# Optimization experiments

Hardware: AMD Instinct MI355X
Metric: run time of the kernel (lower is better)

## Reference

```python
import jax, jax.numpy as jnp
import numpy as np

K = 11  # masked conv3d kernel size

def mask_A(k):
    # mask type 'A': flattened (i,j,t) positions with current_id < k^3//2 + 1
    # (current_id starts at 1) -> first k^3//2 positions are 1.
    m = (np.arange(k ** 3) < (k ** 3) // 2).astype(np.float32).reshape(k, k, k)
    return jnp.asarray(m)

def conv3d(x, w, b, pad):
    out = jax.lax.conv_general_dilated(
        x, w, window_strides=(1, 1, 1), padding=[(pad, pad)] * 3,
        dimension_numbers=('NCDHW', 'OIDHW', 'NCDHW'))
    return out + b[None, :, None, None, None]

def conv2d(x, w, b, pad):
    out = jax.lax.conv_general_dilated(
        x, w, window_strides=(1, 1), padding=[(pad, pad)] * 2,
        dimension_numbers=('NCHW', 'OIHW', 'NCHW'))
    return out + b[None, :, None, None]

def pconv(x, w, b):
    # 1x1x1 conv3d as channel GEMM; w: [O, C]
    return jnp.einsum('bcdhw,oc->bodhw', x, w) + b[None, :, None, None, None]

def _phi(z):
    return 0.5 * (1.0 + jax.lax.erf(z / jnp.sqrt(2.0).astype(z.dtype)))

def setup_inputs() -> dict:
    key = jax.random.key(0)
    ks = jax.random.split(key, 12)
    M = 192
    B, H, W = 1, 48, 48
    s = 0.02
    x = jax.random.normal(ks[0], (B, M, H, W), jnp.float32)
    hyper = jax.random.normal(ks[1], (B, 2 * M, H, W), jnp.float32)
    W3 = s * jax.random.normal(ks[2], (M, 2 * M, 3, 3), jnp.float32)
    b3 = jnp.zeros((M,), jnp.float32)
    W1 = s * jax.random.normal(ks[3], (24, 1, K, K, K), jnp.float32)
    b1 = jnp.zeros((24,), jnp.float32)
    Wa = s * jax.random.normal(ks[4], (48, 25), jnp.float32)
    ba = jnp.zeros((48,), jnp.float32)
    Wb = s * jax.random.normal(ks[5], (96, 48), jnp.float32)
    bb = jnp.zeros((96,), jnp.float32)
    Wc = s * jax.random.normal(ks[6], (9, 96), jnp.float32)
    bc = jnp.zeros((9,), jnp.float32)
    return {"x": x, "hyper": hyper, "W3": W3, "b3": b3, "W1": W1, "b1": b1,
            "Wa": Wa, "ba": ba, "Wb": Wb, "bb": bb, "Wc": Wc, "bc": bc}

def reference(x, hyper, W3, b3, W1, b1, Wa, ba, Wb, bb, Wc, bc):
    # x: [B,M,H,W], hyper: [B,2M,H,W]
    x5 = x[:, None]                                   # [B,1,M,H,W]
    h = conv2d(hyper, W3, b3, 1)[:, None]             # [B,1,M,H,W]
    W1m = W1 * mask_A(K)[None, None]                  # causal mask re-applied each fwd
    x1 = conv3d(x5, W1m, b1, 5)                       # [B,24,M,H,W]
    t = jnp.concatenate([x1, h], axis=1)              # [B,25,M,H,W]
    t = jax.nn.relu(pconv(t, Wa, ba))                 # [B,48,M,H,W]
    t = jax.nn.relu(pconv(t, Wb, bb))                 # [B,96,M,H,W]
    out = pconv(t, Wc, bc)                            # [B,9,M,H,W]
    # 3-component weighted Gaussian entropy model
    mu = out[:, 0:3]
    sc = out[:, 3:6]
    sc = jnp.abs(jnp.where(sc == 0.0, 1e-9, sc))
    w = jax.nn.softmax(out[:, 6:9], axis=1)
    xe = x[:, None]                                   # [B,1,M,H,W]
    lik = jnp.abs(_phi((xe + 0.5 - mu) / sc) - _phi((xe - 0.5 - mu) / sc))
    p3 = jnp.sum(w * lik, axis=1)                     # [B,M,H,W]
    return (p3, out)
```

## Files before the change

kernel.cpp:

```cpp
#include <hip/hip_runtime.h>
#include <hip/hip_fp16.h>
#include <math.h>

#define HW    2304
#define NPOS  442368

typedef _Float16 f16x8 __attribute__((ext_vector_type(8)));
typedef __fp16   h16x2 __attribute__((ext_vector_type(2)));
typedef float    f32x4 __attribute__((ext_vector_type(4)));

__device__ __forceinline__ float phi_f(float z) {
    return 0.5f * (1.0f + erff(z * 0.70710678118654752f));
}
__device__ __forceinline__ unsigned short f2h(float v) {
    _Float16 h = (_Float16)v;
    return *reinterpret_cast<unsigned short*>(&h);
}
__device__ __forceinline__ unsigned int pk2(float a, float b) {
    return (unsigned int)f2h(a) | ((unsigned int)f2h(b) << 16);
}
__device__ __forceinline__ unsigned int pkrtz(float a, float b) {
    h16x2 h = __builtin_amdgcn_cvt_pkrtz(a, b);
    return *reinterpret_cast<unsigned int*>(&h);
}
__device__ __forceinline__ unsigned int bperm(int idx4, unsigned int v) {
    return (unsigned int)__builtin_amdgcn_ds_bpermute(idx4, (int)v);
}

__global__ __launch_bounds__(256) void prep_hyperTp(const float* __restrict__ hyper,
                                                    unsigned short* __restrict__ hyperTp) {
    __shared__ float s[32][33];
    const int bx = blockIdx.x;
    const int pt = bx % 79, it = bx / 79;
    const int tid = threadIdx.x;
    const int c = tid & 31, r = tid >> 5;
    const int pp = pt * 32 + c;
    const int yp = pp / 50, xp = pp % 50;
    const bool inter = (pp < 2500) && yp >= 1 && yp <= 48 && xp >= 1 && xp <= 48;
    const int src = inter ? ((yp - 1) * 48 + (xp - 1)) : 0;
#pragma unroll
    for (int i = 0; i < 4; ++i) {
        int icl = r + i * 8;
        s[icl][c] = inter ? hyper[(size_t)(it * 32 + icl) * HW + src] : 0.f;
    }
    __syncthreads();
#pragma unroll
    for (int i = 0; i < 4; ++i) {
        int pl = r + i * 8;
        int pp2 = pt * 32 + pl;
        if (pp2 < 2500)
            hyperTp[(size_t)pp2 * 384 + it * 32 + c] = f2h(s[c][pl]);
    }
}

__global__ __launch_bounds__(256) void prep_apack(const float* __restrict__ W3,
                                                  unsigned short* __restrict__ apack) {
    int idx = blockIdx.x * 256 + threadIdx.x;
    int j = idx & 7;
    int l = (idx >> 3) & 63;
    int rest = idx >> 9;
    int t = rest % 9; rest /= 9;
    int c = rest % 12; int T = rest / 12;
    int oc = T * 16 + (l & 15);
    int ic = c * 32 + (l >> 4) * 8 + j;
    apack[idx] = f2h(W3[((size_t)oc * 384 + ic) * 9 + t]);
}

__global__ __launch_bounds__(256) void prep_rest(const float* __restrict__ W1,
                                                 const float* __restrict__ Wa,
                                                 const float* __restrict__ ba,
                                                 const float* __restrict__ b1,
                                                 const float* __restrict__ Wb,
                                                 const float* __restrict__ bb,
                                                 const float* __restrict__ Wc,
                                                 const float* __restrict__ xg,
                                                 unsigned short* __restrict__ pk,
                                                 unsigned short* __restrict__ xhp) {
    const int bx = blockIdx.x;
    if (bx < 160) {
        int idx = bx * 256 + threadIdx.x;
        float v = 0.f;
        if (idx < 31744) {
            int j = idx & 7, lane = (idx >> 3) & 63, s = (idx >> 9) & 1, c = idx >> 10;
            int q = lane >> 4;
            int oc = s * 16 + (lane & 15);
            int r = 2 * c + (q >> 1), h = q & 1, kw = 8 * h + j;
            if (oc < 24 && r < 61 && kw < 11) {
                int kd = r / 11, kh = r % 11;
                int tap = kd * 121 + kh * 11 + kw;
                if (tap < 665) v = W1[oc * 1331 + tap];
            }
        } else if (idx < 33280) {
            int i2 = idx - 31744;
            int j = i2 & 7, lane = (i2 >> 3) & 63, t = i2 >> 9;
            int m = t * 16 + (lane & 15), k = (lane >> 4) * 8 + j;
            if (k < 25) v = Wa[m * 25 + k];
            else if (k == 25) {
                float s = ba[m];
                for (int c = 0; c < 24; ++c) s += Wa[m * 25 + c] * b1[c];
                v = s;
            }
        } else if (idx < 39424) {
            int i3 = idx - 33280;
            int j = i3 & 7, lane = (i3 >> 3) & 63, k2 = (i3 >> 9) & 1, s = i3 >> 10;
            int m = s * 16 + (lane & 15), ch = k2 * 32 + (lane >> 4) * 8 + j;
            if (ch < 48) v = Wb[m * 48 + ch];
            else if (ch == 48) v = bb[m];
        } else {
            int i4 = idx - 39424;
            int j = i4 & 7, lane = (i4 >> 3) & 63, k3 = i4 >> 9;
            int m = lane & 15, ch = k3 * 32 + (lane >> 4) * 8 + j;
            if (m < 9) v = Wc[m * 96 + ch];
        }
        pk[idx] = f2h(v);
    } else {
        int idx = (bx - 160) * 256 + threadIdx.x;
        if (idx >= 187456) return;
        int si = idx * 4;
        int zp = si / 3712, rem = si - zp * 3712;
        int yp = rem >> 6, xp0 = rem & 63;
        float f[4];
#pragma unroll
        for (int k = 0; k < 4; ++k) {
            int xp = xp0 + k;
            bool in = zp >= 5 && zp < 197 && yp >= 5 && yp < 53 && xp >= 5 && xp < 53;
            f[k] = in ? xg[(size_t)(zp - 5) * HW + (yp - 5) * 48 + (xp - 5)] : 0.f;
        }
        *(uint2*)&xhp[si] = make_uint2(pk2(f[0], f[1]), pk2(f[2], f[3]));
    }
}

__global__ __launch_bounds__(256, 4) void fused3(const unsigned short* __restrict__ xhp,
                                                 const unsigned short* __restrict__ pk,
                                                 const unsigned short* __restrict__ hyperTp,
                                                 const unsigned short* __restrict__ apack,
                                                 const float* __restrict__ b3,
                                                 const float* __restrict__ xg,
                                                 const float* __restrict__ bc,
                                                 float* __restrict__ out) {
    __shared__ __align__(16) unsigned short P[6656];
    __shared__ __align__(16) float htile[256];
    __shared__ __align__(16) unsigned short WU[9216];

    const int tid = threadIdx.x, w = tid >> 6, lane = tid & 63;
    const int n = lane & 15, q = lane >> 4;
    const int bx = blockIdx.x;
    const int x0 = (bx % 12) * 4, y0 = ((bx / 12) % 12) * 4;
    const int T = bx / 144, d0 = T * 16;

    float* hpart = (float*)WU;

#pragma unroll
    for (int k = 0; k < 3; ++k) {
        int idx = tid + k * 256;
        if (idx < 588) {
            int row = idx >> 1, half = idx & 1;
            int py = row / 21, pz = row - py * 21;
            const uint4* src = (const uint4*)(xhp + ((size_t)(d0 + pz) * 58 + (y0 + py)) * 64
                                              + x0 + half * 8);
            *(uint4*)&P[row * 16 + half * 8] = *src;
        }
    }

    {
        const int pp = (y0 + (n >> 2)) * 50 + x0 + (n & 3);
        const size_t bbase = (size_t)pp * 384 + q * 8;
        f32x4 hc[3];
#pragma unroll
        for (int cc = 0; cc < 3; ++cc) {
            const int c = w * 3 + cc;
            const unsigned short* ap = apack + ((size_t)(T * 12 + c) * 9) * 512 + lane * 8;
            const int coff = c * 32;
            f32x4 a0 = {0.f, 0.f, 0.f, 0.f};
#pragma unroll
            for (int t = 0; t < 9; ++t) {
                f16x8 a = *(const f16x8*)(ap + t * 512);
                const int dd = (t / 3) * 50 + (t % 3);
                f16x8 b = *(const f16x8*)(hyperTp + bbase + (size_t)dd * 384 + coff);
                a0 = __builtin_amdgcn_mfma_f32_16x16x32_f16(a, b, a0, 0, 0, 0);
            }
            hc[cc] = a0;
        }
#pragma unroll
        for (int e = 0; e < 4; ++e)
            hpart[w * 256 + (q * 4 + e) * 16 + n] = hc[0][e] + hc[1][e] + hc[2][e];
    }
    __syncthreads();

    {
        const int oc = tid >> 4, pos = tid & 15;
        float h = b3[d0 + oc];
#pragma unroll
        for (int ww = 0; ww < 4; ++ww) h += hpart[ww * 256 + oc * 16 + pos];
        htile[oc * 16 + pos] = h;
    }

    const uint4* pkW4 = (const uint4*)(pk + 31744);
    uint4 wreg[4], wreg4;
#pragma unroll
    for (int k = 0; k < 4; ++k) wreg[k] = pkW4[tid + k * 256];
    wreg4 = (tid < 128) ? pkW4[tid + 1024] : make_uint4(0u, 0u, 0u, 0u);

    const f32x4 zf = {0.f, 0.f, 0.f, 0.f};
    f32x4 acc[4][2];
#pragma unroll
    for (int p = 0; p < 4; ++p) { acc[p][0] = zf; acc[p][1] = zf; }

    const f16x8* Av = (const f16x8*)pk;
    const int par = q >> 1;
    const unsigned short* Pb = P + (w * 21 + n) * 16 + (q & 1) * 8;
#pragma unroll
    for (int c = 0; c < 31; ++c) {
        const int r0 = 2 * c, r1 = 2 * c + 1;
        const int o0 = ((r0 % 11) * 21 + (r0 / 11)) * 16;
        const int o1 = ((r1 % 11) * 21 + (r1 / 11)) * 16;
        const unsigned short* rp = Pb + (par ? o1 : o0);
        unsigned int u[6];
        *(uint4*)&u[0] = *(const uint4*)rp;
        *(uint2*)&u[4] = *(const uint2*)(rp + 8);
        f16x8 ca0 = Av[c * 128 + lane];
        f16x8 ca1 = Av[c * 128 + 64 + lane];
#pragma unroll
        for (int px = 0; px < 4; ++px) {
            unsigned int bw[4];
#pragma unroll
            for (int i = 0; i < 4; ++i) {
                if ((px & 1) == 0) bw[i] = u[(px >> 1) + i];
                else bw[i] = (u[(px >> 1) + i] >> 16) | (u[(px >> 1) + 1 + i] << 16);
            }
            f16x8 bf = *(f16x8*)bw;
            acc[px][0] = __builtin_amdgcn_mfma_f32_16x16x32_f16(ca0, bf, acc[px][0], 0, 0, 0);
            acc[px][1] = __builtin_amdgcn_mfma_f32_16x16x32_f16(ca1, bf, acc[px][1], 0, 0, 0);
        }
    }
    __syncthreads();

#pragma unroll
    for (int px = 0; px < 4; ++px) {
        unsigned int lo = pk2(acc[px][0][0], acc[px][0][1]);
        unsigned int hi = pk2(acc[px][0][2], acc[px][0][3]);
        *(uint2*)&P[(w * 16 + n) * 104 + px * 24 + q * 4] = make_uint2(lo, hi);
        if (q < 2) {
            unsigned int l2 = pk2(acc[px][1][0], acc[px][1][1]);
            unsigned int h2 = pk2(acc[px][1][2], acc[px][1][3]);
            *(uint2*)&P[(w * 16 + n) * 104 + px * 24 + 16 + q * 4] = make_uint2(l2, h2);
        }
    }
    {
        uint4* WU4 = (uint4*)WU;
#pragma unroll
        for (int k = 0; k < 4; ++k) WU4[tid + k * 256] = wreg[k];
        if (tid < 128) WU4[tid + 1024] = wreg4;
    }
    __syncthreads();

    const unsigned short* WaL = WU;
    const unsigned short* WbL = WU + 1536;
    const unsigned short* WcL = WU + 7680;
    float bcv[4];
#pragma unroll
    for (int e = 0; e < 4; ++e) bcv[e] = (q * 4 + e < 9) ? bc[q * 4 + e] : 0.f;

    const int idxg[2] = { (n + 16 * ((2 * q + 0) & 3)) * 4,
                          (n + 16 * ((2 * q + 1) & 3)) * 4 };
    const bool qlo = (q < 2);

    const f16x8 z8 = {};
    for (int px = 0; px < 4; ++px) {
        f16x8 b0;
        if (q < 3) {
            b0 = *(const f16x8*)&P[(w * 16 + n) * 104 + px * 24 + q * 8];
        } else {
            b0 = z8;
            b0[0] = (_Float16)htile[n * 16 + w * 4 + px];
            b0[1] = (_Float16)1.0f;
        }
        unsigned int pw1[6];
#pragma unroll
        for (int s = 0; s < 3; ++s) {
            f16x8 a = *(const f16x8*)&WaL[(s * 64 + lane) * 8];
            f32x4 r1 = __builtin_amdgcn_mfma_f32_16x16x32_f16(a, b0, zf, 0, 0, 0);
            pw1[s * 2 + 0] = pkrtz(fmaxf(r1[0], 0.f), fmaxf(r1[1], 0.f));
            pw1[s * 2 + 1] = pkrtz(fmaxf(r1[2], 0.f), fmaxf(r1[3], 0.f));
        }
        unsigned int bpA[3][2][2];
#pragma unroll
        for (int s = 0; s < 3; ++s)
#pragma unroll
            for (int h = 0; h < 2; ++h) {
                bpA[s][h][0] = bperm(idxg[0], pw1[s * 2 + h]);
                bpA[s][h][1] = bperm(idxg[1], pw1[s * 2 + h]);
            }
        unsigned int bf0w[4], bf1w[4];
#pragma unroll
        for (int ww = 0; ww < 4; ++ww) {
            const int h = ww & 1, g = ww >> 1;
            bf0w[ww] = qlo ? bpA[0][h][g] : bpA[1][h][g];
            unsigned int c1 = (q == 2) ? ((ww == 0) ? 0x00003C00u : 0u) : 0u;
            bf1w[ww] = qlo ? bpA[2][h][g] : c1;
        }
        f16x8 bf0 = *(f16x8*)bf0w, bf1 = *(f16x8*)bf1w;
        unsigned int pw2[12];
#pragma unroll
        for (int s = 0; s < 6; ++s) {
            f16x8 a0w = *(const f16x8*)&WbL[((s * 2 + 0) * 64 + lane) * 8];
            f16x8 a1w = *(const f16x8*)&WbL[((s * 2 + 1) * 64 + lane) * 8];
            f32x4 rb = __builtin_amdgcn_mfma_f32_16x16x32_f16(a0w, bf0, zf, 0, 0, 0);
            rb = __builtin_amdgcn_mfma_f32_16x16x32_f16(a1w, bf1, rb, 0, 0, 0);
            pw2[s * 2 + 0] = pkrtz(fmaxf(rb[0], 0.f), fmaxf(rb[1], 0.f));
            pw2[s * 2 + 1] = pkrtz(fmaxf(rb[2], 0.f), fmaxf(rb[3], 0.f));
        }
        f32x4 rc = zf;
#pragma unroll
        for (int k3 = 0; k3 < 3; ++k3) {
            unsigned int wv[4];
#pragma unroll
            for (int ww = 0; ww < 4; ++ww) {
                const int h = ww & 1, g = ww >> 1;
                unsigned int lo_ = bperm(idxg[g], pw2[(2 * k3) * 2 + h]);
                unsigned int hi_ = bperm(idxg[g], pw2[(2 * k3 + 1) * 2 + h]);
                wv[ww] = qlo ? lo_ : hi_;
            }
            f16x8 bfc = *(f16x8*)wv;
            f16x8 aw = *(const f16x8*)&WcL[(k3 * 64 + lane) * 8];
            rc = __builtin_amdgcn_mfma_f32_16x16x32_f16(aw, bfc, rc, 0, 0, 0);
        }
        {
            float* pr = (float*)(P + (w * 16 + n) * 104 + px * 24);
#pragma unroll
            for (int e = 0; e < 4; ++e) {
                const int row = q * 4 + e;
                if (row < 9) pr[row] = rc[e] + bcv[e];
            }
        }
    }

    {
        const float* pr = (const float*)(P + (w * 16 + (lane >> 2)) * 104 + (lane & 3) * 24);
        f32x4 oA = *(const f32x4*)pr;
        f32x4 oB = *(const f32x4*)(pr + 4);
        float o8 = pr[8];
        const int gp = (d0 + (lane >> 2)) * HW + (y0 + w) * 48 + x0 + (lane & 3);
        const float xv = xg[gp];
        float m = fmaxf(oB[2], fmaxf(oB[3], o8));
        float e0 = expf(oB[2] - m), e1 = expf(oB[3] - m), e2 = expf(o8 - m);
        float inv_es = 1.0f / (e0 + e1 + e2);
        float mu0 = oA[0], mu1 = oA[1], mu2 = oA[2];
        float s0 = oA[3], s1 = oB[0], s2 = oB[1];
        float p = 0.f;
#pragma unroll
        for (int jj = 0; jj < 3; ++jj) {
            float mu = (jj == 0) ? mu0 : (jj == 1) ? mu1 : mu2;
            float sc = (jj == 0) ? s0 : (jj == 1) ? s1 : s2;
            sc = (sc == 0.0f) ? 1e-9f : sc;
            sc = fabsf(sc);
            float a = phi_f((xv + 0.5f - mu) / sc);
            float b = phi_f((xv - 0.5f - mu) / sc);
            float lik = fabsf(a - b);
            float wgt = ((jj == 0) ? e0 : (jj == 1) ? e1 : e2) * inv_es;
            p = fmaf(wgt, lik, p);
        }
        out[gp] = p;
        out[NPOS + (size_t)0 * NPOS + gp] = mu0;
        out[NPOS + (size_t)1 * NPOS + gp] = mu1;
        out[NPOS + (size_t)2 * NPOS + gp] = mu2;
        out[NPOS + (size_t)3 * NPOS + gp] = s0;
        out[NPOS + (size_t)4 * NPOS + gp] = s1;
        out[NPOS + (size_t)5 * NPOS + gp] = s2;
        out[NPOS + (size_t)6 * NPOS + gp] = oB[2];
        out[NPOS + (size_t)7 * NPOS + gp] = oB[3];
        out[NPOS + (size_t)8 * NPOS + gp] = o8;
    }
}

extern "C" void kernel_launch(void* const* d_in, const int* in_sizes, int n_in,
                              void* d_out, int out_size, void* d_ws, size_t ws_size,
                              hipStream_t stream) {
    const float* x     = (const float*)d_in[0];
    const float* hyper = (const float*)d_in[1];
    const float* W3    = (const float*)d_in[2];
    const float* b3    = (const float*)d_in[3];
    const float* W1    = (const float*)d_in[4];
    const float* b1    = (const float*)d_in[5];
    const float* Wa    = (const float*)d_in[6];
    const float* ba    = (const float*)d_in[7];
    const float* Wb    = (const float*)d_in[8];
    const float* bb    = (const float*)d_in[9];
    const float* Wc    = (const float*)d_in[10];
    const float* bc    = (const float*)d_in[11];
    float* out = (float*)d_out;

    unsigned short* hyperTp = (unsigned short*)d_ws;
    unsigned short* apack   = hyperTp + 960000;
    unsigned short* pk      = apack + 663552;
    unsigned short* xhp     = pk + 40960;

    prep_hyperTp<<<948, 256, 0, stream>>>(hyper, hyperTp);
    prep_apack<<<2592, 256, 0, stream>>>(W3, apack);
    prep_rest<<<893, 256, 0, stream>>>(W1, Wa, ba, b1, Wb, bb, Wc, x, pk, xhp);
    fused3<<<1728, 256, 0, stream>>>(xhp, pk, hyperTp, apack, b3, x, bc, out);
}
```

Measured before the change: 160.2 us.

## Merge prep kernels into one launch and async-load MLP weights to LDS

The three preprocessing kernels become a single prep_all launch that dispatches on block index, removing two kernel launches and their gaps. In fused3, the MLP weights are copied directly into LDS with global_load_lds at kernel start instead of being staged through registers and stored after the conv loop. hpart gets its own shared buffer so it no longer aliases WU, and one __syncthreads is dropped. This raises LDS use per block, which may reduce occupancy, and it relies on earlier barriers to make the async LDS loads visible before they are read.

Measured after the change: 154.2 us. -3.8%, faster.

```diff
diff --git a/kernel.cpp b/kernel.cpp
--- a/kernel.cpp
+++ b/kernel.cpp
@@ -26,59 +26,62 @@
 __device__ __forceinline__ unsigned int bperm(int idx4, unsigned int v) {
     return (unsigned int)__builtin_amdgcn_ds_bpermute(idx4, (int)v);
 }
-
-__global__ __launch_bounds__(256) void prep_hyperTp(const float* __restrict__ hyper,
-                                                    unsigned short* __restrict__ hyperTp) {
-    __shared__ float s[32][33];
+__device__ __forceinline__ void gll16(const unsigned short* g, unsigned short* l) {
+    __builtin_amdgcn_global_load_lds(
+        (const __attribute__((address_space(1))) unsigned int*)g,
+        (__attribute__((address_space(3))) unsigned int*)l, 16, 0, 0);
+}
+
+__global__ __launch_bounds__(256) void prep_all(const float* __restrict__ hyper,
+                                                const float* __restrict__ W3,
+                                                const float* __restrict__ W1,
+                                                const float* __restrict__ Wa,
+                                                const float* __restrict__ ba,
+                                                const float* __restrict__ b1,
+                                                const float* __restrict__ Wb,
+                                                const float* __restrict__ bb,
+                                                const float* __restrict__ Wc,
+                                                const float* __restrict__ xg,
+                                                unsigned short* __restrict__ hyperTp,
+                                                unsigned short* __restrict__ apack,
+                                                unsigned short* __restrict__ pk,
+                                                unsigned short* __restrict__ xhp) {
     const int bx = blockIdx.x;
-    const int pt = bx % 79, it = bx / 79;
-    const int tid = threadIdx.x;
-    const int c = tid & 31, r = tid >> 5;
-    const int pp = pt * 32 + c;
-    const int yp = pp / 50, xp = pp % 50;
-    const bool inter = (pp < 2500) && yp >= 1 && yp <= 48 && xp >= 1 && xp <= 48;
-    const int src = inter ? ((yp - 1) * 48 + (xp - 1)) : 0;
-#pragma unroll
-    for (int i = 0; i < 4; ++i) {
-        int icl = r + i * 8;
-        s[icl][c] = inter ? hyper[(size_t)(it * 32 + icl) * HW + src] : 0.f;
-    }
-    __syncthreads();
-#pragma unroll
-    for (int i = 0; i < 4; ++i) {
-        int pl = r + i * 8;
-        int pp2 = pt * 32 + pl;
-        if (pp2 < 2500)
-            hyperTp[(size_t)pp2 * 384 + it * 32 + c] = f2h(s[c][pl]);
-    }
-}
-
-__global__ __launch_bounds__(256) void prep_apack(const float* __restrict__ W3,
-                                                  unsigned short* __restrict__ apack) {
-    int idx = blockIdx.x * 256 + threadIdx.x;
-    int j = idx & 7;
-    int l = (idx >> 3) & 63;
-    int rest = idx >> 9;
-    int t = rest % 9; rest /= 9;
-    int c = rest % 12; int T = rest / 12;
-    int oc = T * 16 + (l & 15);
-    int ic = c * 32 + (l >> 4) * 8 + j;
-    apack[idx] = f2h(W3[((size_t)oc * 384 + ic) * 9 + t]);
-}
-
-__global__ __launch_bounds__(256) void prep_rest(const float* __restrict__ W1,
-                                                 const float* __restrict__ Wa,
-                                                 const float* __restrict__ ba,
-                                                 const float* __restrict__ b1,
-                                                 const float* __restrict__ Wb,
-                                                 const float* __restrict__ bb,
-                                                 const float* __restrict__ Wc,
-                                                 const float* __restrict__ xg,
-                                                 unsigned short* __restrict__ pk,
-                                                 unsigned short* __restrict__ xhp) {
-    const int bx = blockIdx.x;
-    if (bx < 160) {
-        int idx = bx * 256 + threadIdx.x;
+    if (bx < 948) {
+        __shared__ float s[32][33];
+        const int pt = bx % 79, it = bx / 79;
+        const int tid = threadIdx.x;
+        const int c = tid & 31, r = tid >> 5;
+        const int pp = pt * 32 + c;
+        const int yp = pp / 50, xp = pp % 50;
+        const bool inter = (pp < 2500) && yp >= 1 && yp <= 48 && xp >= 1 && xp <= 48;
+        const int src = inter ? ((yp - 1) * 48 + (xp - 1)) : 0;
+#pragma unroll
+        for (int i = 0; i < 4; ++i) {
+            int icl = r + i * 8;
+            s[icl][c] = inter ? hyper[(size_t)(it * 32 + icl) * HW + src] : 0.f;
+        }
+        __syncthreads();
+#pragma unroll
+        for (int i = 0; i < 4; ++i) {
+            int pl = r + i * 8;
+            int pp2 = pt * 32 + pl;
+            if (pp2 < 2500)
+                hyperTp[(size_t)pp2 * 384 + it * 32 + c] = f2h(s[c][pl]);
+        }
+    } else if (bx < 3540) {
+        int idx = (bx - 948) * 256 + threadIdx.x;
+        int j = idx & 7;
+        int l = (idx >> 3) & 63;
+        int rest = idx >> 9;
+        int t = rest % 9; rest /= 9;
+        int c = rest % 12; int T = rest / 12;
+        int oc = T * 16 + (l & 15);
+        int ic = c * 32 + (l >> 4) * 8 + j;
+        apack[idx] = f2h(W3[((size_t)oc * 384 + ic) * 9 + t]);
+    } else if (bx < 3700) {
+        int idx = (bx - 3540) * 256 + threadIdx.x;
+        if (idx >= 40960) return;
         float v = 0.f;
         if (idx < 31744) {
             int j = idx & 7, lane = (idx >> 3) & 63, s = (idx >> 9) & 1, c = idx >> 10;
@@ -114,7 +117,7 @@
         }
         pk[idx] = f2h(v);
     } else {
-        int idx = (bx - 160) * 256 + threadIdx.x;
+        int idx = (bx - 3700) * 256 + threadIdx.x;
         if (idx >= 187456) return;
         int si = idx * 4;
         int zp = si / 3712, rem = si - zp * 3712;
@@ -140,6 +143,7 @@
                                                  float* __restrict__ out) {
     __shared__ __align__(16) unsigned short P[6656];
     __shared__ __align__(16) float htile[256];
+    __shared__ __align__(16) float hpart[1024];
     __shared__ __align__(16) unsigned short WU[9216];
 
     const int tid = threadIdx.x, w = tid >> 6, lane = tid & 63;
@@ -148,7 +152,12 @@
     const int x0 = (bx % 12) * 4, y0 = ((bx / 12) % 12) * 4;
     const int T = bx / 144, d0 = T * 16;
 
-    float* hpart = (float*)WU;
+#pragma unroll
+    for (int k = 0; k < 5; ++k) {
+        int s = w + k * 4;
+        if (s < 18)
+            gll16(pk + 31744 + s * 512 + lane * 8, WU + s * 512);
+    }
 
 #pragma unroll
     for (int k = 0; k < 3; ++k) {
@@ -194,12 +203,6 @@
         for (int ww = 0; ww < 4; ++ww) h += hpart[ww * 256 + oc * 16 + pos];
         htile[oc * 16 + pos] = h;
     }
-
-    const uint4* pkW4 = (const uint4*)(pk + 31744);
-    uint4 wreg[4], wreg4;
-#pragma unroll
-    for (int k = 0; k < 4; ++k) wreg[k] = pkW4[tid + k * 256];
-    wreg4 = (tid < 128) ? pkW4[tid + 1024] : make_uint4(0u, 0u, 0u, 0u);
 
     const f32x4 zf = {0.f, 0.f, 0.f, 0.f};
     f32x4 acc[4][2];
@@ -246,13 +249,6 @@
             *(uint2*)&P[(w * 16 + n) * 104 + px * 24 + 16 + q * 4] = make_uint2(l2, h2);
         }
     }
-    {
-        uint4* WU4 = (uint4*)WU;
-#pragma unroll
-        for (int k = 0; k < 4; ++k) WU4[tid + k * 256] = wreg[k];
-        if (tid < 128) WU4[tid + 1024] = wreg4;
-    }
-    __syncthreads();
 
     const unsigned short* WaL = WU;
     const unsigned short* WbL = WU + 1536;
@@ -395,8 +391,7 @@
     unsigned short* pk      = apack + 663552;
     unsigned short* xhp     = pk + 40960;
 
-    prep_hyperTp<<<948, 256, 0, stream>>>(hyper, hyperTp);
-    prep_apack<<<2592, 256, 0, stream>>>(W3, apack);
-    prep_rest<<<893, 256, 0, stream>>>(W1, Wa, ba, b1, Wb, bb, Wc, x, pk, xhp);
+    prep_all<<<4433, 256, 0, stream>>>(hyper, W3, W1, Wa, ba, b1, Wb, bb, Wc, x,
+                                       hyperTp, apack, pk, xhp);
     fused3<<<1728, 256, 0, stream>>>(xhp, pk, hyperTp, apack, b3, x, bc, out);
 }
```
